# Kernel tuning notes

Hardware: AMD Instinct MI355X
Metric: run time of the kernel (lower is better)

## Reference

```python
import jax, jax.numpy as jnp
import numpy as np

GROUP_SIZE = 32
OUT_FEATURES = 4096
IN_FEATURES = 4096


def _unpack_3bit(p):
    # p: [..., 3] uint8 -> [..., 8] 3-bit values in [0, 7]
    b0, b1, b2 = p[..., 0], p[..., 1], p[..., 2]
    v0 = b0 & 7
    v1 = (b0 >> 3) & 7
    v2 = ((b0 >> 6) & 3) | ((b1 & 1) << 2)
    v3 = (b1 >> 1) & 7
    v4 = (b1 >> 4) & 7
    v5 = ((b1 >> 7) & 1) | ((b2 & 3) << 1)
    v6 = (b2 >> 2) & 7
    v7 = (b2 >> 5) & 7
    return jnp.stack([v0, v1, v2, v3, v4, v5, v6, v7], axis=-1)


def _block_dequantize_3bit(packed, normalization, group_size=GROUP_SIZE):
    # packed: [n_groups, group_size*3//8] int8, normalization: [n_groups, 1]
    p = packed.astype(jnp.uint8).reshape(-1, group_size // 8, 3)
    q = _unpack_3bit(p).reshape(-1, group_size).astype(jnp.float32)
    n = normalization.astype(jnp.float32)  # [n_groups, 1]
    x_norm = q / 7.0
    return (x_norm * (2.0 * n) - n).reshape(-1)


def setup_inputs() -> dict:
    key = jax.random.key(0)
    k1, k2, k3, k4 = jax.random.split(key, 4)
    n_groups = OUT_FEATURES * IN_FEATURES // GROUP_SIZE
    packed_cols = GROUP_SIZE * 3 // 8
    x = jax.random.normal(k1, (2, 2048, IN_FEATURES), dtype=jnp.float32)
    weight_q3 = jax.random.randint(k2, (n_groups, packed_cols), 0, 256, dtype=jnp.int32).astype(jnp.int8)
    weight_norm = jax.random.uniform(k3, (n_groups, 1), dtype=jnp.float32, minval=0.05, maxval=1.0)
    bias = jax.random.normal(k4, (OUT_FEATURES,), dtype=jnp.float32) * 0.02
    return {"x": x, "weight_q3": weight_q3, "weight_norm": weight_norm, "bias": bias}


def reference(x, weight_q3, weight_norm, bias):
    # Dequantize 3-bit packed weights to fp32 [out, in], then F.linear.
    w = _block_dequantize_3bit(weight_q3, weight_norm).reshape(OUT_FEATURES, IN_FEATURES)
    return jnp.einsum('bsi,oi->bso', x, w) + bias
```

## Files before the change

### kernel.cpp

```cpp
#include <hip/hip_runtime.h>
#include <hip/hip_bf16.h>
#include <stdint.h>

#define OUTF 4096
#define INF  4096
#define MROWS 4096
#define GS 32

typedef __attribute__((ext_vector_type(8))) __bf16 bf16x8;
typedef __attribute__((ext_vector_type(4))) float f32x4;

__device__ inline void gload_lds16(const void* g, void* l) {
    __builtin_amdgcn_global_load_lds(
        (const __attribute__((address_space(1))) void*)g,
        (__attribute__((address_space(3))) void*)l, 16, 0, 0);
}

__global__ void cvt_x_kernel(const float* __restrict__ x, __bf16* __restrict__ xb, int n8) {
    int i = blockIdx.x * blockDim.x + threadIdx.x;
    if (i >= n8) return;
    const f32x4* xp = (const f32x4*)x;
    f32x4 a = xp[2 * i], b = xp[2 * i + 1];
    bf16x8 v = { (__bf16)a[0], (__bf16)a[1], (__bf16)a[2], (__bf16)a[3],
                 (__bf16)b[0], (__bf16)b[1], (__bf16)b[2], (__bf16)b[3] };
    ((bf16x8*)xb)[i] = v;
}

__device__ inline void load_group_bits(const int* __restrict__ wq, int gid,
                                       uint64_t& lo, uint64_t& hi) {
    const int4* p = (const int4*)(wq + (size_t)gid * 12);
    int4 A = p[0], B = p[1], C = p[2];
    uint32_t d0 = (uint32_t)(A.x & 255) | ((uint32_t)(A.y & 255) << 8) |
                  ((uint32_t)(A.z & 255) << 16) | ((uint32_t)(A.w & 255) << 24);
    uint32_t d1 = (uint32_t)(B.x & 255) | ((uint32_t)(B.y & 255) << 8) |
                  ((uint32_t)(B.z & 255) << 16) | ((uint32_t)(B.w & 255) << 24);
    uint32_t d2 = (uint32_t)(C.x & 255) | ((uint32_t)(C.y & 255) << 8) |
                  ((uint32_t)(C.z & 255) << 16) | ((uint32_t)(C.w & 255) << 24);
    lo = (uint64_t)d0 | ((uint64_t)d1 << 32);
    hi = (uint64_t)d1 | ((uint64_t)d2 << 32);
}

__global__ void dequant_w_kernel(const int* __restrict__ wq,
                                 const float* __restrict__ wn,
                                 __bf16* __restrict__ wb) {
    int gid = blockIdx.x * blockDim.x + threadIdx.x;
    uint64_t lo, hi;
    load_group_bits(wq, gid, lo, hi);
    float nrm = wn[gid];
    float c2 = nrm * (2.0f / 7.0f), c1 = -nrm;
    bf16x8 o[4];
#pragma unroll
    for (int j = 0; j < 32; ++j) {
        uint32_t q = (j <= 20) ? (uint32_t)((lo >> (3 * j)) & 7)
                               : (uint32_t)((hi >> (3 * j - 32)) & 7);
        o[j >> 3][j & 7] = (__bf16)((float)q * c2 + c1);
    }
    bf16x8* outp = (bf16x8*)(wb + (size_t)gid * 32);
    outp[0] = o[0]; outp[1] = o[1]; outp[2] = o[2]; outp[3] = o[3];
}

template <bool PRE>
__global__ __launch_bounds__(256, 2) void gemm_kernel(
    const float* __restrict__ x, const __bf16* __restrict__ xb,
    const int* __restrict__ wq, const float* __restrict__ wn,
    const __bf16* __restrict__ wb, const float* __restrict__ bias,
    float* __restrict__ out) {
    __shared__ __align__(16) unsigned char lAraw[128 * 128];
    __shared__ __align__(16) unsigned char lBraw[128 * 128];

    const int tid = threadIdx.x;
    const int lane = tid & 63, wid = tid >> 6;
    const int wr = wid >> 1, wc = wid & 1;
    const int bn = blockIdx.x, bm = blockIdx.y;
    const int row16 = lane & 15, kq = lane >> 4;

    f32x4 acc[4][4] = {};

    int aoff[4], boff[4];
#pragma unroll
    for (int m = 0; m < 4; ++m) {
        int r = wr * 64 + m * 16 + row16;
        aoff[m] = r * 128 + ((kq * 16) ^ ((r & 7) << 4));
    }
#pragma unroll
    for (int n = 0; n < 4; ++n) {
        int r = wc * 64 + n * 16 + row16;
        boff[n] = r * 128 + ((kq * 16) ^ ((r & 7) << 4));
    }

    const int srow = lane >> 3;
    const int schunk = (lane & 7) ^ (srow & 7);

    for (int kt = 0; kt < INF / 64; ++kt) {
        __syncthreads();
        if (PRE) {
#pragma unroll
            for (int it = 0; it < 4; ++it) {
                int seg = wid * 4 + it;
                int row = seg * 8 + srow;
                const char* src = (const char*)xb +
                    ((size_t)(bm * 128 + row) * INF + kt * 64 + schunk * 8) * 2;
                gload_lds16(src, lAraw + seg * 1024);
            }
#pragma unroll
            for (int it = 0; it < 4; ++it) {
                int seg = wid * 4 + it;
                int row = seg * 8 + srow;
                const char* src = (const char*)wb +
                    ((size_t)(bn * 128 + row) * INF + kt * 64 + schunk * 8) * 2;
                gload_lds16(src, lBraw + seg * 1024);
            }
        } else {
#pragma unroll
            for (int it = 0; it < 4; ++it) {
                int row = it * 32 + (tid >> 3), c = tid & 7;
                const f32x4* xp = (const f32x4*)(x + (size_t)(bm * 128 + row) * INF + kt * 64 + c * 8);
                f32x4 a0 = xp[0], a1 = xp[1];
                bf16x8 v = { (__bf16)a0[0], (__bf16)a0[1], (__bf16)a0[2], (__bf16)a0[3],
                             (__bf16)a1[0], (__bf16)a1[1], (__bf16)a1[2], (__bf16)a1[3] };
                *(bf16x8*)(lAraw + row * 128 + ((c * 16) ^ ((row & 7) << 4))) = v;
            }
            int row = tid >> 1, gi = tid & 1;
            int gid = (bn * 128 + row) * (INF / GS) + kt * 2 + gi;
            uint64_t lo, hi;
            load_group_bits(wq, gid, lo, hi);
            float nrm = wn[gid];
            float c2 = nrm * (2.0f / 7.0f), c1 = -nrm;
            bf16x8 o[4];
#pragma unroll
            for (int j = 0; j < 32; ++j) {
                uint32_t q = (j <= 20) ? (uint32_t)((lo >> (3 * j)) & 7)
                                       : (uint32_t)((hi >> (3 * j - 32)) & 7);
                o[j >> 3][j & 7] = (__bf16)((float)q * c2 + c1);
            }
            unsigned swz = (row & 7) << 4;
#pragma unroll
            for (int c4 = 0; c4 < 4; ++c4)
                *(bf16x8*)(lBraw + row * 128 + ((gi * 64 + c4 * 16) ^ swz)) = o[c4];
        }
        __syncthreads();

#pragma unroll
        for (int kk = 0; kk < 2; ++kk) {
            bf16x8 af[4], bff[4];
#pragma unroll
            for (int m = 0; m < 4; ++m)
                af[m] = *(const bf16x8*)(lAraw + (aoff[m] ^ (kk * 64)));
#pragma unroll
            for (int n = 0; n < 4; ++n)
                bff[n] = *(const bf16x8*)(lBraw + (boff[n] ^ (kk * 64)));
#pragma unroll
            for (int m = 0; m < 4; ++m)
#pragma unroll
                for (int n = 0; n < 4; ++n)
                    acc[m][n] = __builtin_amdgcn_mfma_f32_16x16x32_bf16(af[m], bff[n], acc[m][n], 0, 0, 0);
        }
    }

#pragma unroll
    for (int n = 0; n < 4; ++n) {
        int col = bn * 128 + wc * 64 + n * 16 + row16;
        float bv = bias[col];
#pragma unroll
        for (int m = 0; m < 4; ++m) {
            int rbase = bm * 128 + wr * 64 + m * 16 + kq * 4;
#pragma unroll
            for (int j = 0; j < 4; ++j)
                out[(size_t)(rbase + j) * OUTF + col] = acc[m][n][j] + bv;
        }
    }
}

extern "C" void kernel_launch(void* const* d_in, const int* in_sizes, int n_in,
                              void* d_out, int out_size, void* d_ws, size_t ws_size,
                              hipStream_t stream) {
    const float* x    = (const float*)d_in[0];
    const int*   wq   = (const int*)d_in[1];
    const float* wn   = (const float*)d_in[2];
    const float* bias = (const float*)d_in[3];
    float* out = (float*)d_out;

    const size_t xb_bytes = (size_t)MROWS * INF * 2;
    const size_t wb_bytes = (size_t)OUTF * INF * 2;
    if (ws_size >= xb_bytes + wb_bytes) {
        __bf16* xb = (__bf16*)d_ws;
        __bf16* wb = (__bf16*)((char*)d_ws + xb_bytes);
        cvt_x_kernel<<<(MROWS * INF / 8 + 255) / 256, 256, 0, stream>>>(x, xb, MROWS * INF / 8);
        dequant_w_kernel<<<(OUTF * INF / GS) / 256, 256, 0, stream>>>(wq, wn, wb);
        gemm_kernel<true><<<dim3(OUTF / 128, MROWS / 128), 256, 0, stream>>>(
            x, xb, wq, wn, wb, bias, out);
    } else {
        gemm_kernel<false><<<dim3(OUTF / 128, MROWS / 128), 256, 0, stream>>>(
            x, nullptr, wq, wn, nullptr, bias, out);
    }
}
```

Measured before the change: 160.9 us.

## Replace bf16 GEMM with 256x256-tile 8-wave double-buffered pipelined kernel

The main GEMM path now uses a 512-thread kernel with 256x256 output tiles, split into four 128x128 quadrants. Global-to-LDS loads of the next k-tile are double-buffered and interleaved with MFMA work on the current one, using explicit vmcnt waits, raw barriers and s_setprio around MFMA bursts. A block-index remap groups workgroups for L2 locality. This targets memory latency and low data reuse of the 128x128 single-buffered kernel, at the cost of 128KB of LDS, which limits occupancy, and more complex synchronisation.

```diff
diff --git a/kernel.cpp b/kernel.cpp
--- a/kernel.cpp
+++ b/kernel.cpp
@@ -59,11 +59,121 @@
     outp[0] = o[0]; outp[1] = o[1]; outp[2] = o[2]; outp[3] = o[3];
 }
 
-template <bool PRE>
-__global__ __launch_bounds__(256, 2) void gemm_kernel(
-    const float* __restrict__ x, const __bf16* __restrict__ xb,
-    const int* __restrict__ wq, const float* __restrict__ wn,
-    const __bf16* __restrict__ wb, const float* __restrict__ bias,
+
+#define VMCNT(N) asm volatile("s_waitcnt vmcnt(" #N ")" ::: "memory")
+#define BARR() do { asm volatile("" ::: "memory"); __builtin_amdgcn_s_barrier(); \
+                    asm volatile("" ::: "memory"); } while (0)
+
+#define LOADA(RB, H) do { \
+    _Pragma("unroll") \
+    for (int m_ = 0; m_ < 4; ++m_) { \
+        const int r_ = wr * 64 + m_ * 16 + row16; \
+        _Pragma("unroll") \
+        for (int kk_ = 0; kk_ < 2; ++kk_) \
+            af[m_][kk_] = *(const bf16x8*)(lds + (RB) * 65536 + (H) * 16384 + \
+                r_ * 128 + (((kk_ * 4 + kq) * 16) ^ ((r_ & 7) << 4))); \
+    } \
+} while (0)
+
+#define LOADB(RB, H) do { \
+    _Pragma("unroll") \
+    for (int n_ = 0; n_ < 2; ++n_) { \
+        const int r_ = wc * 32 + n_ * 16 + row16; \
+        _Pragma("unroll") \
+        for (int kk_ = 0; kk_ < 2; ++kk_) \
+            bf[n_][kk_] = *(const bf16x8*)(lds + (RB) * 65536 + 32768 + (H) * 16384 + \
+                r_ * 128 + (((kk_ * 4 + kq) * 16) ^ ((r_ & 7) << 4))); \
+    } \
+} while (0)
+
+#define STAGEA(SB, H, SKT) do { \
+    _Pragma("unroll") \
+    for (int j_ = 0; j_ < 2; ++j_) \
+        gload_lds16((const char*)(xb + (size_t)(bm * 256 + (H) * 128 + j_ * 64 + srow) * INF + \
+                                  (SKT) * 64 + schunk * 8), \
+                    lds + (SB) * 65536 + (H) * 16384 + j_ * 8192 + tid * 16); \
+} while (0)
+
+#define STAGEB(SB, H, SKT) do { \
+    _Pragma("unroll") \
+    for (int j_ = 0; j_ < 2; ++j_) \
+        gload_lds16((const char*)(wb + (size_t)(bn * 256 + (H) * 128 + j_ * 64 + srow) * INF + \
+                                  (SKT) * 64 + schunk * 8), \
+                    lds + (SB) * 65536 + 32768 + (H) * 16384 + j_ * 8192 + tid * 16); \
+} while (0)
+
+#define MFMA16(MH, NH) do { \
+    __builtin_amdgcn_s_setprio(1); \
+    _Pragma("unroll") \
+    for (int kk_ = 0; kk_ < 2; ++kk_) \
+        _Pragma("unroll") \
+        for (int m_ = 0; m_ < 4; ++m_) \
+            _Pragma("unroll") \
+            for (int n_ = 0; n_ < 2; ++n_) \
+                acc[MH][NH][m_][n_] = __builtin_amdgcn_mfma_f32_16x16x32_bf16( \
+                    af[m_][kk_], bf[n_][kk_], acc[MH][NH][m_][n_], 0, 0, 0); \
+    __builtin_amdgcn_s_setprio(0); \
+} while (0)
+
+#define HALF_ITER(RB, SB, SKT) do { \
+    LOADA(RB, 0); LOADB(RB, 0); STAGEA(SB, 0, SKT); VMCNT(2); BARR(); MFMA16(0, 0); BARR(); \
+    LOADB(RB, 1);               STAGEB(SB, 0, SKT);           BARR(); MFMA16(0, 1); BARR(); \
+    LOADA(RB, 1);               STAGEA(SB, 1, SKT);           BARR(); MFMA16(1, 1); BARR(); \
+    LOADB(RB, 0);               STAGEB(SB, 1, SKT); VMCNT(4); BARR(); MFMA16(1, 0); BARR(); \
+} while (0)
+
+__global__ __launch_bounds__(512, 2) void gemm8_kernel(
+    const __bf16* __restrict__ xb, const __bf16* __restrict__ wb,
+    const float* __restrict__ bias, float* __restrict__ out) {
+    __shared__ __align__(16) unsigned char lds[131072];
+
+    const int tid = threadIdx.x;
+    const int lane = tid & 63, wid = tid >> 6;
+    const int wr = wid >> 2, wc = wid & 3;
+    const int row16 = lane & 15, kq = lane >> 4;
+
+    const int bid = blockIdx.x;
+    const int wg = (bid & 7) * 32 + (bid >> 3);
+    const int bn = wg & 15, bm = wg >> 4;
+
+    const int srow = tid >> 3;
+    const int schunk = (tid & 7) ^ (srow & 7);
+
+    f32x4 acc[2][2][4][2] = {};
+    bf16x8 af[4][2], bf[2][2];
+
+    STAGEA(0, 0, 0); STAGEB(0, 0, 0); STAGEA(0, 1, 0); STAGEB(0, 1, 0);
+    VMCNT(4);
+    BARR();
+
+    for (int kt = 0; kt < INF / 64; kt += 2) {
+        const int s1 = kt + 1;
+        const int s2 = (kt + 2) & 63;
+        HALF_ITER(0, 1, s1);
+        HALF_ITER(1, 0, s2);
+    }
+
+#pragma unroll
+    for (int nh = 0; nh < 2; ++nh)
+#pragma unroll
+        for (int n = 0; n < 2; ++n) {
+            const int col = bn * 256 + nh * 128 + wc * 32 + n * 16 + row16;
+            const float bv = bias[col];
+#pragma unroll
+            for (int mh = 0; mh < 2; ++mh)
+#pragma unroll
+                for (int m = 0; m < 4; ++m) {
+                    const int rbase = bm * 256 + mh * 128 + wr * 64 + m * 16 + kq * 4;
+#pragma unroll
+                    for (int j = 0; j < 4; ++j)
+                        out[(size_t)(rbase + j) * OUTF + col] = acc[mh][nh][m][n][j] + bv;
+                }
+        }
+}
+
+__global__ __launch_bounds__(256, 2) void gemm_fb_kernel(
+    const float* __restrict__ x, const int* __restrict__ wq,
+    const float* __restrict__ wn, const float* __restrict__ bias,
     float* __restrict__ out) {
     __shared__ __align__(16) unsigned char lAraw[128 * 128];
     __shared__ __align__(16) unsigned char lBraw[128 * 128];
@@ -88,38 +198,18 @@
         boff[n] = r * 128 + ((kq * 16) ^ ((r & 7) << 4));
     }
 
-    const int srow = lane >> 3;
-    const int schunk = (lane & 7) ^ (srow & 7);
-
     for (int kt = 0; kt < INF / 64; ++kt) {
         __syncthreads();
-        if (PRE) {
-#pragma unroll
-            for (int it = 0; it < 4; ++it) {
-                int seg = wid * 4 + it;
-                int row = seg * 8 + srow;
-                const char* src = (const char*)xb +
-                    ((size_t)(bm * 128 + row) * INF + kt * 64 + schunk * 8) * 2;
-                gload_lds16(src, lAraw + seg * 1024);
-            }
-#pragma unroll
-            for (int it = 0; it < 4; ++it) {
-                int seg = wid * 4 + it;
-                int row = seg * 8 + srow;
-                const char* src = (const char*)wb +
-                    ((size_t)(bn * 128 + row) * INF + kt * 64 + schunk * 8) * 2;
-                gload_lds16(src, lBraw + seg * 1024);
-            }
-        } else {
-#pragma unroll
-            for (int it = 0; it < 4; ++it) {
-                int row = it * 32 + (tid >> 3), c = tid & 7;
-                const f32x4* xp = (const f32x4*)(x + (size_t)(bm * 128 + row) * INF + kt * 64 + c * 8);
-                f32x4 a0 = xp[0], a1 = xp[1];
-                bf16x8 v = { (__bf16)a0[0], (__bf16)a0[1], (__bf16)a0[2], (__bf16)a0[3],
-                             (__bf16)a1[0], (__bf16)a1[1], (__bf16)a1[2], (__bf16)a1[3] };
-                *(bf16x8*)(lAraw + row * 128 + ((c * 16) ^ ((row & 7) << 4))) = v;
-            }
+#pragma unroll
+        for (int it = 0; it < 4; ++it) {
+            int row = it * 32 + (tid >> 3), c = tid & 7;
+            const f32x4* xp = (const f32x4*)(x + (size_t)(bm * 128 + row) * INF + kt * 64 + c * 8);
+            f32x4 a0 = xp[0], a1 = xp[1];
+            bf16x8 v = { (__bf16)a0[0], (__bf16)a0[1], (__bf16)a0[2], (__bf16)a0[3],
+                         (__bf16)a1[0], (__bf16)a1[1], (__bf16)a1[2], (__bf16)a1[3] };
+            *(bf16x8*)(lAraw + row * 128 + ((c * 16) ^ ((row & 7) << 4))) = v;
+        }
+        {
             int row = tid >> 1, gi = tid & 1;
             int gid = (bn * 128 + row) * (INF / GS) + kt * 2 + gi;
             uint64_t lo, hi;
@@ -142,18 +232,18 @@
 
 #pragma unroll
         for (int kk = 0; kk < 2; ++kk) {
-            bf16x8 af[4], bff[4];
+            bf16x8 afr[4], bfr[4];
 #pragma unroll
             for (int m = 0; m < 4; ++m)
-                af[m] = *(const bf16x8*)(lAraw + (aoff[m] ^ (kk * 64)));
+                afr[m] = *(const bf16x8*)(lAraw + (aoff[m] ^ (kk * 64)));
 #pragma unroll
             for (int n = 0; n < 4; ++n)
-                bff[n] = *(const bf16x8*)(lBraw + (boff[n] ^ (kk * 64)));
+                bfr[n] = *(const bf16x8*)(lBraw + (boff[n] ^ (kk * 64)));
 #pragma unroll
             for (int m = 0; m < 4; ++m)
 #pragma unroll
                 for (int n = 0; n < 4; ++n)
-                    acc[m][n] = __builtin_amdgcn_mfma_f32_16x16x32_bf16(af[m], bff[n], acc[m][n], 0, 0, 0);
+                    acc[m][n] = __builtin_amdgcn_mfma_f32_16x16x32_bf16(afr[m], bfr[n], acc[m][n], 0, 0, 0);
         }
     }
 
@@ -187,10 +277,8 @@
         __bf16* wb = (__bf16*)((char*)d_ws + xb_bytes);
         cvt_x_kernel<<<(MROWS * INF / 8 + 255) / 256, 256, 0, stream>>>(x, xb, MROWS * INF / 8);
         dequant_w_kernel<<<(OUTF * INF / GS) / 256, 256, 0, stream>>>(wq, wn, wb);
-        gemm_kernel<true><<<dim3(OUTF / 128, MROWS / 128), 256, 0, stream>>>(
-            x, xb, wq, wn, wb, bias, out);
+        gemm8_kernel<<<(MROWS / 256) * (OUTF / 256), 512, 0, stream>>>(xb, wb, bias, out);
     } else {
-        gemm_kernel<false><<<dim3(OUTF / 128, MROWS / 128), 256, 0, stream>>>(
-            x, nullptr, wq, wn, nullptr, bias, out);
-    }
-}
+        gemm_fb_kernel<<<dim3(OUTF / 128, MROWS / 128), 256, 0, stream>>>(x, wq, wn, bias, out);
+    }
+}
```

Measured after the change: 142.4 us. -11.5%, faster.
